# Kernel tuning notes

Measured on AMD Instinct MI355X. Metric: run time of the kernel, lower is better.

Reference implementation:

```python
import jax, jax.numpy as jnp
import numpy as np

B, S, H, DK = 64, 8192, 8, 8  # d_k must equal n_wires=8 (encoder maps feature i -> RX on wire i)
E = H * DK                    # embed_dim = 64


def _quantum_heads(x, theta):
    """Exact closed form of the 8-wire circuit per (batch, token, head).

    Circuit: RX(x_i) then trainable RX(theta_i) on each wire i (RX(a)RX(b)=RX(a+b)),
    CNOT chain (0->1, 1->2, ..., 6->7, 7->0), then <Z_w> on every wire.
    Starting from |0..0>, the post-RX state is a product state with per-wire
    bit probabilities p(1)=sin^2(a_i/2); CNOTs classically permute basis states:
    bit_k' = XOR(b_0..b_k) for k>=1 and bit_0' = XOR(b_1..b_7). Since the bits are
    independent with E[(-1)^{b_j}] = cos(a_j):
        <Z_0> = prod_{j=1..7} cos(a_j)
        <Z_k> = prod_{j=0..k} cos(a_j)   (k >= 1)
    This equals the full statevector simulation exactly.
    """
    a = x.reshape(B, S, H, DK) + theta            # angles, [B,S,H,8]
    c = jnp.cos(a)
    cp = jnp.cumprod(c, axis=-1)                  # <Z_k> for k>=1 is cp[..., k]
    z0 = jnp.prod(c[..., 1:], axis=-1, keepdims=True)
    return jnp.concatenate([z0, cp[..., 1:]], axis=-1)  # [B,S,H,8]


def setup_inputs() -> dict:
    key = jax.random.key(0)
    k1, k2, k3, k4 = jax.random.split(key, 4)
    lim = 1.0 / float(np.sqrt(E))
    return {
        "x": jax.random.normal(k1, (B, S, E), jnp.float32),
        "theta": jax.random.normal(k2, (DK,), jnp.float32),
        "w_combine": jax.random.uniform(k3, (E, E), jnp.float32, -lim, lim),
        "b_combine": jax.random.uniform(k4, (E,), jnp.float32, -lim, lim),
    }


def reference(x, theta, w_combine, b_combine):
    # q, k, v are all the SAME quantum projection of the SAME x in the original.
    z = _quantum_heads(x, theta)                              # [B,S,H,DK]
    # torch matmul on [B,S,H,DK]: attention is across the HEAD axis per token.
    scores = jnp.einsum('bshd,bstd->bsht', z, z) * (DK ** -0.5)
    attn = jax.nn.softmax(scores, axis=-1)                    # dropout: eval mode (identity)
    out = jnp.einsum('bsht,bstd->bshd', attn, z)              # [B,S,H,DK]
    # matches torch .transpose(1,2).contiguous().view(B, -1, E)
    out = out.transpose(0, 2, 1, 3).reshape(B, S, E)
    return out @ w_combine.T + b_combine
```

## Files before the change

### kernel.cpp

```cpp
#include <hip/hip_runtime.h>

typedef __attribute__((ext_vector_type(8))) short bf16x8;
typedef __attribute__((ext_vector_type(4))) float f32x4;

template <int CTRL>
__device__ __forceinline__ float qperm(float x) {
    return __builtin_bit_cast(float,
        __builtin_amdgcn_update_dpp(0, __builtin_bit_cast(int, x), CTRL, 0xf, 0xf, true));
}

__global__ __launch_bounds__(256) void qattn(const float* __restrict__ x,
                                             const float* __restrict__ theta,
                                             const float* __restrict__ wc,
                                             const float* __restrict__ bc,
                                             float* __restrict__ out)
{
    __shared__ __align__(16) unsigned short sWhi[512 * 8];
    __shared__ __align__(16) unsigned short sWlo[512 * 8];

    const int tid = threadIdx.x;
    #pragma unroll
    for (int f0 = 0; f0 < 2; ++f0) {
        const int f = tid * 2 + f0;
        const int snt = f >> 6, ln = f & 63;
        const int s = snt >> 2, nt = snt & 3;
        const int r = nt * 16 + (ln & 15);
        const int koff = s * 32 + (ln >> 4) * 8;
        const float* wp = wc + r * 64 + koff;
        float w8[8];
        *(float4*)(&w8[0]) = *(const float4*)(wp);
        *(float4*)(&w8[4]) = *(const float4*)(wp + 4);
        #pragma unroll
        for (int j = 0; j < 8; ++j) {
            unsigned u = __builtin_bit_cast(unsigned, w8[j]);
            sWhi[f * 8 + j] = (unsigned short)(u >> 16);
            float rhi = __builtin_bit_cast(float, u & 0xffff0000u);
            unsigned l = __builtin_bit_cast(unsigned, w8[j] - rhi);
            sWlo[f * 8 + j] = (unsigned short)(l >> 16);
        }
    }
    __syncthreads();

    const int lane = tid & 63;
    const int wid  = tid >> 6;
    const int h    = lane & 7;
    const int G1   = (lane >> 3) & 1;
    const int kch  = lane >> 4;
    const int col  = lane & 15;
    const int fby  = lane * 8;

    float th[8];
    #pragma unroll
    for (int d = 0; d < 8; ++d) th[d] = theta[d];
    float bs[4];
    #pragma unroll
    for (int nt = 0; nt < 4; ++nt) bs[nt] = bc[nt * 16 + col];

    const int P0 = (int)blockIdx.x * 4 + wid;
    const float* xp0 = x + ((size_t)((2 * P0 + G1) * 8 + kch)) * 64 + h * 8;
    const size_t IT_STRIDE = (size_t)8192 * 16 * 64;

    float4 cur[4];
    cur[0] = *(const float4*)(xp0);
    cur[1] = *(const float4*)(xp0 + 4);
    cur[2] = *(const float4*)(xp0 + 256);
    cur[3] = *(const float4*)(xp0 + 260);

    #pragma unroll
    for (int it = 0; it < 4; ++it) {
        float4 nxt[4];
        if (it < 3) {
            const float* p = xp0 + (size_t)(it + 1) * IT_STRIDE;
            nxt[0] = *(const float4*)(p);
            nxt[1] = *(const float4*)(p + 4);
            nxt[2] = *(const float4*)(p + 256);
            nxt[3] = *(const float4*)(p + 260);
        }

        const int P = it * 8192 + P0;

        bf16x8 ahi[2], alo[2];
        #pragma unroll
        for (int s = 0; s < 2; ++s) {
            float v[8];
            *(float4*)(&v[0]) = cur[s * 2 + 0];
            *(float4*)(&v[4]) = cur[s * 2 + 1];

            float c[8];
            #pragma unroll
            for (int d = 0; d < 8; ++d) c[d] = __cosf(v[d] + th[d]);

            float z[8];
            z[1] = c[0] * c[1];
            #pragma unroll
            for (int d = 2; d < 8; ++d) z[d] = z[d - 1] * c[d];
            float p = c[1];
            #pragma unroll
            for (int d = 2; d < 8; ++d) p *= c[d];
            z[0] = p;

            float z7[8];
            #pragma unroll
            for (int d = 0; d < 8; ++d) z7[d] = qperm<0x141>(z[d]);

            float osum[8];
            #pragma unroll
            for (int d = 0; d < 8; ++d) osum[d] = 0.f;
            float esum = 0.f;

            #define QSTEP(ZT0,ZT1,ZT2,ZT3,ZT4,ZT5,ZT6,ZT7)                         \
                do {                                                               \
                    float zt_[8] = {ZT0,ZT1,ZT2,ZT3,ZT4,ZT5,ZT6,ZT7};              \
                    float sc = zt_[0] * z[0];                                      \
                    _Pragma("unroll")                                              \
                    for (int d = 1; d < 8; ++d) sc = fmaf(zt_[d], z[d], sc);       \
                    float e = __builtin_amdgcn_exp2f(0.51006978f * sc);            \
                    esum += e;                                                     \
                    _Pragma("unroll")                                              \
                    for (int d = 0; d < 8; ++d) osum[d] = fmaf(e, zt_[d], osum[d]);\
                } while (0)

            QSTEP(z[0],z[1],z[2],z[3],z[4],z[5],z[6],z[7]);
            {
                float t0[8], t1[8], t2[8];
                #pragma unroll
                for (int d = 0; d < 8; ++d) t0[d] = qperm<0xB1>(z[d]);
                QSTEP(t0[0],t0[1],t0[2],t0[3],t0[4],t0[5],t0[6],t0[7]);
                #pragma unroll
                for (int d = 0; d < 8; ++d) t1[d] = qperm<0x4E>(z[d]);
                QSTEP(t1[0],t1[1],t1[2],t1[3],t1[4],t1[5],t1[6],t1[7]);
                #pragma unroll
                for (int d = 0; d < 8; ++d) t2[d] = qperm<0x1B>(z[d]);
                QSTEP(t2[0],t2[1],t2[2],t2[3],t2[4],t2[5],t2[6],t2[7]);
            }
            QSTEP(z7[0],z7[1],z7[2],z7[3],z7[4],z7[5],z7[6],z7[7]);
            {
                float t0[8], t1[8], t2[8];
                #pragma unroll
                for (int d = 0; d < 8; ++d) t0[d] = qperm<0xB1>(z7[d]);
                QSTEP(t0[0],t0[1],t0[2],t0[3],t0[4],t0[5],t0[6],t0[7]);
                #pragma unroll
                for (int d = 0; d < 8; ++d) t1[d] = qperm<0x4E>(z7[d]);
                QSTEP(t1[0],t1[1],t1[2],t1[3],t1[4],t1[5],t1[6],t1[7]);
                #pragma unroll
                for (int d = 0; d < 8; ++d) t2[d] = qperm<0x1B>(z7[d]);
                QSTEP(t2[0],t2[1],t2[2],t2[3],t2[4],t2[5],t2[6],t2[7]);
            }
            #undef QSTEP

            float r = __builtin_amdgcn_rcpf(esum);
            float o[8];
            #pragma unroll
            for (int d = 0; d < 8; ++d) o[d] = osum[d] * r;

            unsigned hp[4], lp[4];
            #pragma unroll
            for (int pq = 0; pq < 4; ++pq) {
                unsigned e0 = __builtin_bit_cast(unsigned, o[2 * pq]);
                unsigned e1 = __builtin_bit_cast(unsigned, o[2 * pq + 1]);
                hp[pq] = (e0 >> 16) | (e1 & 0xffff0000u);
                float r0 = __builtin_bit_cast(float, e0 & 0xffff0000u);
                float r1 = __builtin_bit_cast(float, e1 & 0xffff0000u);
                unsigned l0 = __builtin_bit_cast(unsigned, o[2 * pq] - r0);
                unsigned l1 = __builtin_bit_cast(unsigned, o[2 * pq + 1] - r1);
                lp[pq] = (l0 >> 16) | (l1 & 0xffff0000u);
            }
            ahi[s] = __builtin_bit_cast(bf16x8, *(const unsigned(*)[4])hp);
            alo[s] = __builtin_bit_cast(bf16x8, *(const unsigned(*)[4])lp);
        }

        #pragma unroll
        for (int q = 0; q < 4; ++q) cur[q] = nxt[q];

        f32x4 acc[4];
        #pragma unroll
        for (int nt = 0; nt < 4; ++nt) acc[nt] = (f32x4){0.f, 0.f, 0.f, 0.f};
        #pragma unroll
        for (int nt = 0; nt < 4; ++nt) {
            #pragma unroll
            for (int s = 0; s < 2; ++s) {
                const int off = (s * 4 + nt) * 512 + fby;
                bf16x8 bhi = *(const bf16x8*)(&sWhi[off]);
                bf16x8 blo = *(const bf16x8*)(&sWlo[off]);
                acc[nt] = __builtin_amdgcn_mfma_f32_16x16x32_bf16(ahi[s], bhi, acc[nt], 0, 0, 0);
                acc[nt] = __builtin_amdgcn_mfma_f32_16x16x32_bf16(alo[s], bhi, acc[nt], 0, 0, 0);
                acc[nt] = __builtin_amdgcn_mfma_f32_16x16x32_bf16(ahi[s], blo, acc[nt], 0, 0, 0);
            }
        }

        #pragma unroll
        for (int q = 0; q < 4; ++q) {
            const int r16 = kch * 4 + q;
            const int hh = r16 & 7;
            const int gg = r16 >> 3;
            const int gf2 = 2 * P + gg;
            const int orow = (gf2 >> 10) * 8192 + hh * 1024 + (gf2 & 1023);
            float* op = out + orow * 64 + col;
            #pragma unroll
            for (int nt = 0; nt < 4; ++nt)
                op[nt * 16] = acc[nt][q] + bs[nt];
        }
    }
}

extern "C" void kernel_launch(void* const* d_in, const int* in_sizes, int n_in,
                              void* d_out, int out_size, void* d_ws, size_t ws_size,
                              hipStream_t stream) {
    const float* x     = (const float*)d_in[0];
    const float* theta = (const float*)d_in[1];
    const float* wc    = (const float*)d_in[2];
    const float* bc    = (const float*)d_in[3];
    float* out = (float*)d_out;
    qattn<<<dim3(2048), dim3(256), 0, stream>>>(x, theta, wc, bc, out);
}
```

Measured before the change: 52.12 us.

## Fold softmax scale into z and weights, use packed FMA and raw cos

Folds the softmax scale (1/sqrt(8)·log2e) into the z values by scaling c[1] by its square root, and undoes it by pre-dividing the combine weights. This removes the per-score multiply before exp2. Computes cos with the hardware cos on fract(angle/2π), which drops __cosf's range handling. Rewrites the score and accumulation loops on float2 vectors so the compiler can emit packed FMAs. Doubles the grid and halves the per-thread iteration count for more parallelism. The scale folding changes how rounding falls in the bf16 hi/lo split, and the raw hardware cos may lose accuracy for large angles.

```diff
diff --git a/kernel.cpp b/kernel.cpp
--- a/kernel.cpp
+++ b/kernel.cpp
@@ -2,11 +2,23 @@
 
 typedef __attribute__((ext_vector_type(8))) short bf16x8;
 typedef __attribute__((ext_vector_type(4))) float f32x4;
+typedef __attribute__((ext_vector_type(2))) float f32x2;
+
+__device__ __forceinline__ f32x2 fma2(f32x2 a, f32x2 b, f32x2 c) {
+    return __builtin_elementwise_fma(a, b, c);
+}
 
 template <int CTRL>
 __device__ __forceinline__ float qperm(float x) {
     return __builtin_bit_cast(float,
         __builtin_amdgcn_update_dpp(0, __builtin_bit_cast(int, x), CTRL, 0xf, 0xf, true));
+}
+template <int CTRL>
+__device__ __forceinline__ f32x2 qperm2(f32x2 x) {
+    f32x2 r;
+    r.x = qperm<CTRL>(x.x);
+    r.y = qperm<CTRL>(x.y);
+    return r;
 }
 
 __global__ __launch_bounds__(256) void qattn(const float* __restrict__ x,
@@ -17,6 +29,10 @@
 {
     __shared__ __align__(16) unsigned short sWhi[512 * 8];
     __shared__ __align__(16) unsigned short sWlo[512 * 8];
+
+    const float KAPPA = 0.71419161f;
+    const float INVK  = 1.40018590f;
+    const float INV2PI = 0.15915494309189535f;
 
     const int tid = threadIdx.x;
     #pragma unroll
@@ -32,10 +48,11 @@
         *(float4*)(&w8[4]) = *(const float4*)(wp + 4);
         #pragma unroll
         for (int j = 0; j < 8; ++j) {
-            unsigned u = __builtin_bit_cast(unsigned, w8[j]);
+            float w = w8[j] * INVK;
+            unsigned u = __builtin_bit_cast(unsigned, w);
             sWhi[f * 8 + j] = (unsigned short)(u >> 16);
             float rhi = __builtin_bit_cast(float, u & 0xffff0000u);
-            unsigned l = __builtin_bit_cast(unsigned, w8[j] - rhi);
+            unsigned l = __builtin_bit_cast(unsigned, w - rhi);
             sWlo[f * 8 + j] = (unsigned short)(l >> 16);
         }
     }
@@ -49,16 +66,19 @@
     const int col  = lane & 15;
     const int fby  = lane * 8;
 
-    float th[8];
-    #pragma unroll
-    for (int d = 0; d < 8; ++d) th[d] = theta[d];
+    f32x2 th2p[4];
+    #pragma unroll
+    for (int j = 0; j < 4; ++j) {
+        th2p[j].x = theta[2 * j] * INV2PI;
+        th2p[j].y = theta[2 * j + 1] * INV2PI;
+    }
     float bs[4];
     #pragma unroll
     for (int nt = 0; nt < 4; ++nt) bs[nt] = bc[nt * 16 + col];
 
     const int P0 = (int)blockIdx.x * 4 + wid;
     const float* xp0 = x + ((size_t)((2 * P0 + G1) * 8 + kch)) * 64 + h * 8;
-    const size_t IT_STRIDE = (size_t)8192 * 16 * 64;
+    const size_t IT_STRIDE = (size_t)16384 * 16 * 64;
 
     float4 cur[4];
     cur[0] = *(const float4*)(xp0);
@@ -67,28 +87,31 @@
     cur[3] = *(const float4*)(xp0 + 260);
 
     #pragma unroll
-    for (int it = 0; it < 4; ++it) {
+    for (int it = 0; it < 2; ++it) {
         float4 nxt[4];
-        if (it < 3) {
-            const float* p = xp0 + (size_t)(it + 1) * IT_STRIDE;
+        if (it < 1) {
+            const float* p = xp0 + IT_STRIDE;
             nxt[0] = *(const float4*)(p);
             nxt[1] = *(const float4*)(p + 4);
             nxt[2] = *(const float4*)(p + 256);
             nxt[3] = *(const float4*)(p + 260);
         }
 
-        const int P = it * 8192 + P0;
+        const int P = it * 16384 + P0;
 
         bf16x8 ahi[2], alo[2];
         #pragma unroll
         for (int s = 0; s < 2; ++s) {
-            float v[8];
-            *(float4*)(&v[0]) = cur[s * 2 + 0];
-            *(float4*)(&v[4]) = cur[s * 2 + 1];
-
+            const f32x2* v2 = (const f32x2*)&cur[s * 2];
+            f32x2 inv2 = {INV2PI, INV2PI};
             float c[8];
             #pragma unroll
-            for (int d = 0; d < 8; ++d) c[d] = __cosf(v[d] + th[d]);
+            for (int j = 0; j < 4; ++j) {
+                f32x2 a2 = fma2(v2[j], inv2, th2p[j]);
+                c[2 * j]     = __builtin_amdgcn_cosf(__builtin_amdgcn_fractf(a2.x));
+                c[2 * j + 1] = __builtin_amdgcn_cosf(__builtin_amdgcn_fractf(a2.y));
+            }
+            c[1] *= KAPPA;
 
             float z[8];
             z[1] = c[0] * c[1];
@@ -99,70 +122,77 @@
             for (int d = 2; d < 8; ++d) p *= c[d];
             z[0] = p;
 
-            float z7[8];
-            #pragma unroll
-            for (int d = 0; d < 8; ++d) z7[d] = qperm<0x141>(z[d]);
-
-            float osum[8];
-            #pragma unroll
-            for (int d = 0; d < 8; ++d) osum[d] = 0.f;
+            f32x2 z2[4];
+            #pragma unroll
+            for (int j = 0; j < 4; ++j) { z2[j].x = z[2 * j]; z2[j].y = z[2 * j + 1]; }
+
+            f32x2 z72[4];
+            #pragma unroll
+            for (int j = 0; j < 4; ++j) z72[j] = qperm2<0x141>(z2[j]);
+
+            f32x2 osum2[4];
+            #pragma unroll
+            for (int j = 0; j < 4; ++j) osum2[j] = (f32x2){0.f, 0.f};
             float esum = 0.f;
 
-            #define QSTEP(ZT0,ZT1,ZT2,ZT3,ZT4,ZT5,ZT6,ZT7)                         \
+            #define QSTEP(ZT)                                                      \
                 do {                                                               \
-                    float zt_[8] = {ZT0,ZT1,ZT2,ZT3,ZT4,ZT5,ZT6,ZT7};              \
-                    float sc = zt_[0] * z[0];                                      \
+                    f32x2 s2 = (ZT)[0] * z2[0];                                    \
+                    s2 = fma2((ZT)[1], z2[1], s2);                                 \
+                    s2 = fma2((ZT)[2], z2[2], s2);                                 \
+                    s2 = fma2((ZT)[3], z2[3], s2);                                 \
+                    float e = __builtin_amdgcn_exp2f(s2.x + s2.y);                 \
+                    esum += e;                                                     \
+                    f32x2 e2 = {e, e};                                             \
                     _Pragma("unroll")                                              \
-                    for (int d = 1; d < 8; ++d) sc = fmaf(zt_[d], z[d], sc);       \
-                    float e = __builtin_amdgcn_exp2f(0.51006978f * sc);            \
-                    esum += e;                                                     \
-                    _Pragma("unroll")                                              \
-                    for (int d = 0; d < 8; ++d) osum[d] = fmaf(e, zt_[d], osum[d]);\
+                    for (int j = 0; j < 4; ++j)                                    \
+                        osum2[j] = fma2(e2, (ZT)[j], osum2[j]);                    \
                 } while (0)
 
-            QSTEP(z[0],z[1],z[2],z[3],z[4],z[5],z[6],z[7]);
+            QSTEP(z2);
             {
-                float t0[8], t1[8], t2[8];
-                #pragma unroll
-                for (int d = 0; d < 8; ++d) t0[d] = qperm<0xB1>(z[d]);
-                QSTEP(t0[0],t0[1],t0[2],t0[3],t0[4],t0[5],t0[6],t0[7]);
-                #pragma unroll
-                for (int d = 0; d < 8; ++d) t1[d] = qperm<0x4E>(z[d]);
-                QSTEP(t1[0],t1[1],t1[2],t1[3],t1[4],t1[5],t1[6],t1[7]);
-                #pragma unroll
-                for (int d = 0; d < 8; ++d) t2[d] = qperm<0x1B>(z[d]);
-                QSTEP(t2[0],t2[1],t2[2],t2[3],t2[4],t2[5],t2[6],t2[7]);
-            }
-            QSTEP(z7[0],z7[1],z7[2],z7[3],z7[4],z7[5],z7[6],z7[7]);
+                f32x2 w2[4];
+                #pragma unroll
+                for (int j = 0; j < 4; ++j) w2[j] = qperm2<0xB1>(z2[j]);
+                QSTEP(w2);
+                #pragma unroll
+                for (int j = 0; j < 4; ++j) w2[j] = qperm2<0x4E>(z2[j]);
+                QSTEP(w2);
+                #pragma unroll
+                for (int j = 0; j < 4; ++j) w2[j] = qperm2<0x1B>(z2[j]);
+                QSTEP(w2);
+            }
+            QSTEP(z72);
             {
-                float t0[8], t1[8], t2[8];
-                #pragma unroll
-                for (int d = 0; d < 8; ++d) t0[d] = qperm<0xB1>(z7[d]);
-                QSTEP(t0[0],t0[1],t0[2],t0[3],t0[4],t0[5],t0[6],t0[7]);
-                #pragma unroll
-                for (int d = 0; d < 8; ++d) t1[d] = qperm<0x4E>(z7[d]);
-                QSTEP(t1[0],t1[1],t1[2],t1[3],t1[4],t1[5],t1[6],t1[7]);
-                #pragma unroll
-                for (int d = 0; d < 8; ++d) t2[d] = qperm<0x1B>(z7[d]);
-                QSTEP(t2[0],t2[1],t2[2],t2[3],t2[4],t2[5],t2[6],t2[7]);
+                f32x2 w2[4];
+                #pragma unroll
+                for (int j = 0; j < 4; ++j) w2[j] = qperm2<0xB1>(z72[j]);
+                QSTEP(w2);
+                #pragma unroll
+                for (int j = 0; j < 4; ++j) w2[j] = qperm2<0x4E>(z72[j]);
+                QSTEP(w2);
+                #pragma unroll
+                for (int j = 0; j < 4; ++j) w2[j] = qperm2<0x1B>(z72[j]);
+                QSTEP(w2);
             }
             #undef QSTEP
 
             float r = __builtin_amdgcn_rcpf(esum);
-            float o[8];
-            #pragma unroll
-            for (int d = 0; d < 8; ++d) o[d] = osum[d] * r;
+            f32x2 r2 = {r, r};
+            f32x2 o2[4];
+            #pragma unroll
+            for (int j = 0; j < 4; ++j) o2[j] = osum2[j] * r2;
 
             unsigned hp[4], lp[4];
             #pragma unroll
             for (int pq = 0; pq < 4; ++pq) {
-                unsigned e0 = __builtin_bit_cast(unsigned, o[2 * pq]);
-                unsigned e1 = __builtin_bit_cast(unsigned, o[2 * pq + 1]);
+                unsigned e0 = __builtin_bit_cast(unsigned, o2[pq].x);
+                unsigned e1 = __builtin_bit_cast(unsigned, o2[pq].y);
                 hp[pq] = (e0 >> 16) | (e1 & 0xffff0000u);
                 float r0 = __builtin_bit_cast(float, e0 & 0xffff0000u);
                 float r1 = __builtin_bit_cast(float, e1 & 0xffff0000u);
-                unsigned l0 = __builtin_bit_cast(unsigned, o[2 * pq] - r0);
-                unsigned l1 = __builtin_bit_cast(unsigned, o[2 * pq + 1] - r1);
+                unsigned l0 = __builtin_bit_cast(unsigned, o2[pq].x - r0);
+                unsigned l1 = __builtin_bit_cast(unsigned, o2[pq].y - r1);
                 lp[pq] = (l0 >> 16) | (l1 & 0xffff0000u);
             }
             ahi[s] = __builtin_bit_cast(bf16x8, *(const unsigned(*)[4])hp);
@@ -211,5 +241,5 @@
     const float* wc    = (const float*)d_in[2];
     const float* bc    = (const float*)d_in[3];
     float* out = (float*)d_out;
-    qattn<<<dim3(2048), dim3(256), 0, stream>>>(x, theta, wc, bc, out);
-}
+    qattn<<<dim3(4096), dim3(256), 0, stream>>>(x, theta, wc, bc, out);
+}
```

Result: no change. 52.62 us (+0.9%).
